# Kernel tuning notes

Measured on AMD Instinct MI355X. Metric: run time of the kernel, lower is better.

The kernel has to match this reference:

```python
import jax, jax.numpy as jnp
import numpy as np

KH, KW = 2, 2  # kernel_size; stride == kernel_size (default), pad == 0 for this config

def setup_inputs() -> dict:
    key = jax.random.key(0)
    k1, k2 = jax.random.split(key)
    B, C, H, W = 32, 64, 64, 64
    nH, nW = H // KH, W // KW
    L = nH * nW                     # 1024
    n = KH * KW * C                 # 256 (grouping = in_feature)
    x = jax.random.normal(k1, (B, C, H, W), dtype=jnp.float32)
    stdv = 6.0 / np.sqrt(n * n / 1.0) ** 0.5  # placeholder, recomputed below
    stdv = 6.0 / np.sqrt(float(n * n) / 1.0) if False else 6.0 / np.sqrt(float(n) * float(n) / float(n)) / 1.0
    stdv = 6.0 / np.sqrt(float(n * n))  # numel // L == n*n -> stdv = 6/sqrt(n*n) = 6/n
    weight = jax.random.uniform(k2, (L, n, n), dtype=jnp.float32, minval=-stdv, maxval=stdv)
    bias = jnp.zeros((1, 1, n, L), dtype=jnp.float32)
    return {"x": x, "weight": weight, "bias": bias}

def reference(x, weight, bias):
    # PointConv with kernel=(2,2), stride=(2,2), pad=0, grouping=C.
    B, C, H, W = x.shape
    nH, nW = H // KH, W // KW
    L = nH * nW
    n = C * KH * KW
    # F.unfold (non-overlapping, stride==kernel): channel order (c, kh, kw), L order (ph, pw)
    patches = x.reshape(B, C, nH, KH, nW, KW).transpose(0, 1, 3, 5, 2, 4).reshape(B, n, L)
    p = patches.reshape(B, 1, n, L)  # (B, C//grouping=1, n, L)
    # per-location matmul: distinct [n,n] weight per spatial patch l
    m = jnp.einsum('bcnl,lnp->bcpl', p, weight) + bias  # (B,1,n,L)
    m = m.reshape(B, C, KH, KW, nH, nW)
    # F.fold inverse of the unfold above
    out = m.transpose(0, 1, 4, 2, 5, 3).reshape(B, C, H, W)
    return out
```

## Files before the change

### kernel.cpp

```cpp
#include <hip/hip_runtime.h>


#define B_  32
#define C_  64
#define H_  64
#define W_  64
#define L_  1024
#define N_  256
#define SA  264

typedef __bf16 bf16x8 __attribute__((ext_vector_type(8)));
typedef float  f32x4  __attribute__((ext_vector_type(4)));

__device__ __forceinline__ unsigned short f2bf(float f) {
  unsigned int u = __builtin_bit_cast(unsigned int, f);
  u += 0x7FFFu + ((u >> 16) & 1u);
  return (unsigned short)(u >> 16);
}

__global__ __launch_bounds__(256, 3) void pointconv_kernel(
    const float* __restrict__ x, const float* __restrict__ wgt,
    const float* __restrict__ bias, float* __restrict__ out) {
  __shared__ unsigned short A[B_ * SA];

  const int bid = blockIdx.x;
  const int l  = ((bid & 7) << 7) | (bid >> 3);
  const int ph = l >> 5, pw = l & 31;
  const int h0 = ph * 2, w0 = pw * 2;
  const int tid = threadIdx.x;

  const float* __restrict__ wl = wgt + (size_t)l * (N_ * N_);

  const int lane = tid & 63;
  const int wv   = tid >> 6;
  const int col  = lane & 15;
  const int quad = lane >> 4;

  const float* __restrict__ wp = wl + (quad * 8) * N_ + wv * 64 + col;

  float rb0[4][8], rb1[4][8];

#pragma unroll
  for (int nt = 0; nt < 4; ++nt)
#pragma unroll
    for (int j = 0; j < 8; ++j)
      rb0[nt][j] = wp[j * N_ + nt * 16];
  __builtin_amdgcn_sched_barrier(0);

  {
    const int b  = tid & 31;
    const int c0 = tid >> 5;
#pragma unroll
    for (int i = 0; i < 8; ++i) {
      const int c = c0 + i * 8;
      const float* px = x + (((b * C_ + c) * H_ + h0) * W_ + w0);
      float2 v0 = *(const float2*)px;
      float2 v1 = *(const float2*)(px + W_);
      ushort4 q;
      q.x = f2bf(v0.x); q.y = f2bf(v0.y);
      q.z = f2bf(v1.x); q.w = f2bf(v1.y);
      *(ushort4*)&A[b * SA + c * 4] = q;
    }
  }

  f32x4 acc[2][4];
#pragma unroll
  for (int nt = 0; nt < 4; ++nt) {
    const int p = wv * 64 + nt * 16 + col;
    const float bv = bias[p * L_ + l];
#pragma unroll
    for (int mt = 0; mt < 2; ++mt) {
      acc[mt][nt][0] = bv; acc[mt][nt][1] = bv;
      acc[mt][nt][2] = bv; acc[mt][nt][3] = bv;
    }
  }

  __syncthreads();

#pragma unroll
  for (int s = 0; s < 8; ++s) {
    if (s < 7) {
      const float* np = wp + (s + 1) * 32 * N_;
      if (s & 1) {
#pragma unroll
        for (int nt = 0; nt < 4; ++nt)
#pragma unroll
          for (int j = 0; j < 8; ++j)
            rb0[nt][j] = np[j * N_ + nt * 16];
      } else {
#pragma unroll
        for (int nt = 0; nt < 4; ++nt)
#pragma unroll
          for (int j = 0; j < 8; ++j)
            rb1[nt][j] = np[j * N_ + nt * 16];
      }
    }
    __builtin_amdgcn_sched_barrier(0);

    bf16x8 af[2];
#pragma unroll
    for (int mt = 0; mt < 2; ++mt)
      af[mt] = *(const bf16x8*)&A[(mt * 16 + col) * SA + s * 32 + quad * 8];

#pragma unroll
    for (int nt = 0; nt < 4; ++nt) {
      union { unsigned short u[8]; bf16x8 v; } bu;
#pragma unroll
      for (int j = 0; j < 8; ++j)
        bu.u[j] = f2bf((s & 1) ? rb1[nt][j] : rb0[nt][j]);
#pragma unroll
      for (int mt = 0; mt < 2; ++mt)
        acc[mt][nt] = __builtin_amdgcn_mfma_f32_16x16x32_bf16(
            af[mt], bu.v, acc[mt][nt], 0, 0, 0);
    }
    __builtin_amdgcn_sched_barrier(0);
  }

#pragma unroll
  for (int mt = 0; mt < 2; ++mt) {
#pragma unroll
    for (int nt = 0; nt < 4; ++nt) {
      const int p  = wv * 64 + nt * 16 + col;
      const int c  = p >> 2;
      const int kh = (p >> 1) & 1;
      const int kw = p & 1;
      float* po = out + (((c * H_) + h0 + kh) * W_ + w0 + kw);
#pragma unroll
      for (int r = 0; r < 4; ++r) {
        const int b = mt * 16 + quad * 4 + r;
        po[b * (C_ * H_ * W_)] = acc[mt][nt][r];
      }
    }
  }
}

extern "C" void kernel_launch(void* const* d_in, const int* in_sizes, int n_in,
                              void* d_out, int out_size, void* d_ws, size_t ws_size,
                              hipStream_t stream) {
  const float* x    = (const float*)d_in[0];
  const float* wgt  = (const float*)d_in[1];
  const float* bias = (const float*)d_in[2];
  float* out = (float*)d_out;
  pointconv_kernel<<<dim3(L_), dim3(256), 0, stream>>>(x, wgt, bias, out);
}
```

Measured before the change: 428.3 us.

## Stream weights into LDS via async global_load_lds with 4-stage ring buffer

Replaces register double-buffered weight loads with direct global-to-LDS asynchronous loads into a four-slot ring buffer of 32-row weight slabs, using XOR swizzling to avoid bank conflicts. Input and bias loads are hoisted ahead of the weight prefetch so more memory requests are in flight. Each K-step waits on vmcnt and synchronizes the block around buffer reuse. This uses about 128KB of LDS per block, which forces one block per CU (launch bounds lowered to 1) and trades occupancy for deeper explicit prefetch; the extra barriers add synchronization cost.

Result: no change. 427.9 us (-0.1%).

```diff
diff --git a/kernel.cpp b/kernel.cpp
--- a/kernel.cpp
+++ b/kernel.cpp
@@ -8,6 +8,7 @@
 #define L_  1024
 #define N_  256
 #define SA  264
+#define NBUF 4
 
 typedef __bf16 bf16x8 __attribute__((ext_vector_type(8)));
 typedef float  f32x4  __attribute__((ext_vector_type(4)));
@@ -18,103 +19,114 @@
   return (unsigned short)(u >> 16);
 }
 
-__global__ __launch_bounds__(256, 3) void pointconv_kernel(
+__device__ __forceinline__ void async_ld16(const float* g, float* l) {
+  __builtin_amdgcn_global_load_lds(
+      (const __attribute__((address_space(1))) void*)g,
+      (__attribute__((address_space(3))) void*)l, 16, 0, 0);
+}
+
+__global__ __launch_bounds__(256, 1) void pointconv_kernel(
     const float* __restrict__ x, const float* __restrict__ wgt,
     const float* __restrict__ bias, float* __restrict__ out) {
-  __shared__ unsigned short A[B_ * SA];
+  __shared__ __align__(16)  unsigned short A[B_ * SA];
+  __shared__ __align__(128) float Wb[NBUF][32 * N_];
 
   const int bid = blockIdx.x;
   const int l  = ((bid & 7) << 7) | (bid >> 3);
   const int ph = l >> 5, pw = l & 31;
   const int h0 = ph * 2, w0 = pw * 2;
-  const int tid = threadIdx.x;
-
-  const float* __restrict__ wl = wgt + (size_t)l * (N_ * N_);
-
+  const int tid  = threadIdx.x;
   const int lane = tid & 63;
   const int wv   = tid >> 6;
   const int col  = lane & 15;
   const int quad = lane >> 4;
 
-  const float* __restrict__ wp = wl + (quad * 8) * N_ + wv * 64 + col;
+  const float* __restrict__ wl = wgt + (size_t)l * (N_ * N_);
+  const float* wsrc = wl + (wv * 8) * N_ + ((lane * 4) ^ ((wv & 1) << 4));
 
-  float rb0[4][8], rb1[4][8];
+  const int ub  = tid & 31;
+  const int uc0 = tid >> 5;
+  float2 xv[8][2];
+#pragma unroll
+  for (int i = 0; i < 8; ++i) {
+    const int c = uc0 + i * 8;
+    const float* px = x + (((ub * C_ + c) * H_ + h0) * W_ + w0);
+    xv[i][0] = *(const float2*)px;
+    xv[i][1] = *(const float2*)(px + W_);
+  }
+  float bv[4];
+#pragma unroll
+  for (int nt = 0; nt < 4; ++nt)
+    bv[nt] = bias[(wv * 64 + nt * 16 + col) * L_ + l];
+  __builtin_amdgcn_sched_barrier(0);
 
 #pragma unroll
-  for (int nt = 0; nt < 4; ++nt)
+  for (int ss = 0; ss < NBUF; ++ss)
 #pragma unroll
-    for (int j = 0; j < 8; ++j)
-      rb0[nt][j] = wp[j * N_ + nt * 16];
+    for (int i = 0; i < 8; ++i)
+      async_ld16(wsrc + (ss * 32 + i) * N_, &Wb[ss][(wv * 8 + i) * N_]);
   __builtin_amdgcn_sched_barrier(0);
 
-  {
-    const int b  = tid & 31;
-    const int c0 = tid >> 5;
 #pragma unroll
-    for (int i = 0; i < 8; ++i) {
-      const int c = c0 + i * 8;
-      const float* px = x + (((b * C_ + c) * H_ + h0) * W_ + w0);
-      float2 v0 = *(const float2*)px;
-      float2 v1 = *(const float2*)(px + W_);
-      ushort4 q;
-      q.x = f2bf(v0.x); q.y = f2bf(v0.y);
-      q.z = f2bf(v1.x); q.w = f2bf(v1.y);
-      *(ushort4*)&A[b * SA + c * 4] = q;
-    }
+  for (int i = 0; i < 8; ++i) {
+    const int c = uc0 + i * 8;
+    ushort4 q;
+    q.x = f2bf(xv[i][0].x); q.y = f2bf(xv[i][0].y);
+    q.z = f2bf(xv[i][1].x); q.w = f2bf(xv[i][1].y);
+    *(ushort4*)&A[ub * SA + c * 4] = q;
   }
 
   f32x4 acc[2][4];
 #pragma unroll
-  for (int nt = 0; nt < 4; ++nt) {
-    const int p = wv * 64 + nt * 16 + col;
-    const float bv = bias[p * L_ + l];
+  for (int nt = 0; nt < 4; ++nt)
 #pragma unroll
     for (int mt = 0; mt < 2; ++mt) {
-      acc[mt][nt][0] = bv; acc[mt][nt][1] = bv;
-      acc[mt][nt][2] = bv; acc[mt][nt][3] = bv;
+      acc[mt][nt][0] = bv[nt]; acc[mt][nt][1] = bv[nt];
+      acc[mt][nt][2] = bv[nt]; acc[mt][nt][3] = bv[nt];
     }
+
+  asm volatile("s_waitcnt lgkmcnt(0)" ::: "memory");
+  __builtin_amdgcn_s_barrier();
+
+#define KSTEP(T, VM)                                                           \
+  {                                                                            \
+    asm volatile("s_waitcnt vmcnt(" #VM ")" ::: "memory");                     \
+    __builtin_amdgcn_sched_barrier(0);                                         \
+    __builtin_amdgcn_s_barrier();                                              \
+    bf16x8 af0 = *(const bf16x8*)&A[col * SA + (T) * 32 + quad * 8];           \
+    bf16x8 af1 = *(const bf16x8*)&A[(16 + col) * SA + (T) * 32 + quad * 8];    \
+    const float* wb = &Wb[(T) & (NBUF - 1)][0];                                \
+    _Pragma("unroll")                                                          \
+    for (int nt = 0; nt < 4; ++nt) {                                           \
+      const int pp = (wv * 64 + nt * 16 + col) ^ ((quad & 1) << 4);            \
+      union { unsigned short u[8]; bf16x8 v; } bu;                             \
+      _Pragma("unroll")                                                        \
+      for (int j = 0; j < 8; ++j)                                              \
+        bu.u[j] = f2bf(wb[(quad * 8 + j) * N_ + pp]);                          \
+      acc[0][nt] = __builtin_amdgcn_mfma_f32_16x16x32_bf16(af0, bu.v,          \
+                                                           acc[0][nt], 0, 0, 0); \
+      acc[1][nt] = __builtin_amdgcn_mfma_f32_16x16x32_bf16(af1, bu.v,          \
+                                                           acc[1][nt], 0, 0, 0); \
+    }                                                                          \
+    __builtin_amdgcn_sched_barrier(0);                                         \
+    __builtin_amdgcn_s_barrier();                                              \
+    if ((T) + NBUF < 8) {                                                      \
+      _Pragma("unroll")                                                        \
+      for (int i = 0; i < 8; ++i)                                              \
+        async_ld16(wsrc + (((T) + NBUF) * 32 + i) * N_,                        \
+                   &Wb[(T) & (NBUF - 1)][(wv * 8 + i) * N_]);                  \
+    }                                                                          \
   }
 
-  __syncthreads();
-
-#pragma unroll
-  for (int s = 0; s < 8; ++s) {
-    if (s < 7) {
-      const float* np = wp + (s + 1) * 32 * N_;
-      if (s & 1) {
-#pragma unroll
-        for (int nt = 0; nt < 4; ++nt)
-#pragma unroll
-          for (int j = 0; j < 8; ++j)
-            rb0[nt][j] = np[j * N_ + nt * 16];
-      } else {
-#pragma unroll
-        for (int nt = 0; nt < 4; ++nt)
-#pragma unroll
-          for (int j = 0; j < 8; ++j)
-            rb1[nt][j] = np[j * N_ + nt * 16];
-      }
-    }
-    __builtin_amdgcn_sched_barrier(0);
-
-    bf16x8 af[2];
-#pragma unroll
-    for (int mt = 0; mt < 2; ++mt)
-      af[mt] = *(const bf16x8*)&A[(mt * 16 + col) * SA + s * 32 + quad * 8];
-
-#pragma unroll
-    for (int nt = 0; nt < 4; ++nt) {
-      union { unsigned short u[8]; bf16x8 v; } bu;
-#pragma unroll
-      for (int j = 0; j < 8; ++j)
-        bu.u[j] = f2bf((s & 1) ? rb1[nt][j] : rb0[nt][j]);
-#pragma unroll
-      for (int mt = 0; mt < 2; ++mt)
-        acc[mt][nt] = __builtin_amdgcn_mfma_f32_16x16x32_bf16(
-            af[mt], bu.v, acc[mt][nt], 0, 0, 0);
-    }
-    __builtin_amdgcn_sched_barrier(0);
-  }
+  KSTEP(0, 24)
+  KSTEP(1, 24)
+  KSTEP(2, 24)
+  KSTEP(3, 24)
+  KSTEP(4, 24)
+  KSTEP(5, 16)
+  KSTEP(6, 8)
+  KSTEP(7, 0)
+#undef KSTEP
 
 #pragma unroll
   for (int mt = 0; mt < 2; ++mt) {
```
